# Kernel tuning notes

Measured on AMD Instinct MI355X. Metric: run time of the kernel, lower is better.

Reference implementation:

```python
import jax, jax.numpy as jnp
import numpy as np

B, NPG, FANOUT = 32, 1024, 4       # graphs, nodes per graph, tree fan-out
H = 128                            # x_size == h_size
NUM_LAYERS = 4
A, BCAPS = 8, 8                    # TreeCaps a, b
DCC, N_CLASSES = 16, 50
ROUTING_ITER = 3
TYPE_VOCAB, TOKEN_VOCAB = 1000, 30000
EPS = 1e-10


def _build_forest():
    # parent of node i (i>0) is (i-1)//FANOUT; node 0 is root. Same tree per graph.
    child = np.arange(1, NPG)
    parent = (child - 1) // FANOUT
    pos = ((child - 1) % FANOUT).astype(np.float32)           # position in parent's mailbox
    cnt = np.bincount(parent, minlength=NPG).astype(np.float32)
    k = cnt[parent]                                           # child count of each edge's parent
    denom = np.maximum(k - 1.0, 1.0)
    lw = np.where(k == 1.0, 1.0, (k - 1.0 - pos) / denom).astype(np.float32)
    rw = np.where(k == 1.0, 0.0, pos / denom).astype(np.float32)
    offs = (np.arange(B) * NPG)[:, None]
    src = (child[None, :] + offs).reshape(-1).astype(np.int32)
    dst = (parent[None, :] + offs).reshape(-1).astype(np.int32)
    return src, dst, np.tile(lw, B), np.tile(rw, B), np.tile(cnt > 0, B)


def setup_inputs() -> dict:
    key = jax.random.key(0)
    ks = jax.random.split(key, 9)
    src, dst, lw, rw, has_children = _build_forest()
    N = B * NPG
    u = lambda k, s: jax.random.uniform(k, s, jnp.float32, -0.1, 0.1)
    return {
        "type_ids": jax.random.randint(ks[0], (N,), 0, TYPE_VOCAB, dtype=jnp.int32),
        "token_ids": jax.random.randint(ks[1], (N,), 0, TOKEN_VOCAB, dtype=jnp.int32),
        "src": jnp.asarray(src), "dst": jnp.asarray(dst),
        "lw": jnp.asarray(lw), "rw": jnp.asarray(rw),
        "has_children": jnp.asarray(has_children),
        "type_emb": jax.random.normal(ks[2], (TYPE_VOCAB, H - H // 2), jnp.float32),
        "token_emb": jax.random.normal(ks[3], (TOKEN_VOCAB, H // 2), jnp.float32),
        "W_left": u(ks[4], (NUM_LAYERS, H, H)),
        "W_right": u(ks[5], (NUM_LAYERS, H, H)),
        "W_top": u(ks[6], (NUM_LAYERS, H, H)),
        "b_conv": u(ks[7], (NUM_LAYERS, H)),
        "Wjm": 0.01 * jax.random.normal(ks[8], (A * H, DCC, N_CLASSES, NUM_LAYERS), jnp.float32),
    }


def squash(x, axis=-1):
    sq = jnp.sum(x * x, axis=axis, keepdims=True)
    return x * (sq / (1.0 + sq) / (jnp.sqrt(sq + EPS) + 1e-8))


def _vts_routing(uu):
    # uu: [NPG, H, L]  (one graph's primary capsules)
    l2 = jnp.sum(uu.reshape(NPG, -1) ** 2, axis=1)
    _, top_b = jax.lax.top_k(l2, BCAPS)
    u_i = jax.lax.stop_gradient(uu[top_b].reshape(-1, NUM_LAYERS))  # [BCAPS*H, L]
    _, top_a = jax.lax.top_k(l2, A)
    v_j = uu[top_a].reshape(-1, NUM_LAYERS)                         # [A*H, L]
    alpha = jnp.zeros((BCAPS * H, A * H), uu.dtype)
    for _ in range(ROUTING_ITER):
        alpha = alpha + u_i @ v_j.T
        beta = jax.nn.softmax(alpha, axis=-1)
        v_j = beta.T @ u_i
    return squash(v_j)                                              # [A*H, L]


def _dynamic_routing(SC, Wjm):
    # SC: [B, A*H, L], Wjm: [A*H, DCC, S, L]
    v = jnp.einsum('ncsm,bnm->bnsc', Wjm, SC)
    v_stop = jax.lax.stop_gradient(v)
    delta = jnp.zeros(SC.shape[:2] + (N_CLASSES,), SC.dtype)
    z = None
    for r in range(ROUTING_ITER):
        gamma = jax.nn.softmax(delta, axis=-1)
        vv = v if r == ROUTING_ITER - 1 else v_stop
        z = squash(jnp.einsum('bns,bnsc->bsc', gamma, vv))
        if r < ROUTING_ITER - 1:
            delta = delta + jnp.einsum('bnsc,bsc->bns', v_stop, z)
    return z                                                        # [B, S, DCC]


def reference(type_ids, token_ids, src, dst, lw, rw, has_children,
              type_emb, token_emb, W_left, W_right, W_top, b_conv, Wjm):
    h = jnp.concatenate([type_emb[type_ids], token_emb[token_ids]], axis=1)  # [N, H]
    N = h.shape[0]
    feats = []
    for l in range(NUM_LAYERS):
        ch = h[src]                                                 # [E, H] gather children
        msg = (ch @ W_left[l]) * lw[:, None] + (ch @ W_right[l]) * rw[:, None]
        children = jax.ops.segment_sum(msg, dst, num_segments=N)
        new_h = jax.nn.relu(children + h @ W_top[l] + b_conv[l][None, :])
        h = jnp.where(has_children[:, None], new_h, h)              # leaves keep old h
        feats.append(h)
    layer_feats = jnp.stack(feats, axis=-1)                         # [N, H, L]
    SC = jax.vmap(_vts_routing)(layer_feats.reshape(B, NPG, H, NUM_LAYERS))
    z = _dynamic_routing(SC, Wjm)
    logit = jnp.sqrt(jnp.sum(z * z, axis=-1) + EPS)                 # [B, S]
    return (logit, logit)
```

## Files before the change

kernel.cpp:

```cpp
#include <hip/hip_runtime.h>


#define BG      32
#define NPG     1024
#define HH      128
#define NLAY    4
#define INT_PG  256
#define M_INT   8192
#define NN      32768
#define EPG     1023
#define DCC     16
#define NS      50

__global__ void k_embed(const int* __restrict__ tids, const int* __restrict__ kids,
                        const float* __restrict__ temb, const float* __restrict__ kemb,
                        float* __restrict__ h) {
  int idx = blockIdx.x * 256 + threadIdx.x;
  int n = idx >> 5, c4 = idx & 31;
  float4 v;
  if (c4 < 16) v = *(const float4*)(temb + tids[n] * 64 + c4 * 4);
  else         v = *(const float4*)(kemb + kids[n] * 64 + (c4 - 16) * 4);
  *(float4*)(h + n * 128 + c4 * 4) = v;
}

__global__ void k_gather(const float* __restrict__ h, const int* __restrict__ src,
                         const float* __restrict__ lw, const float* __restrict__ rw,
                         float* __restrict__ hl, float* __restrict__ hr) {
  int idx = blockIdx.x * 256 + threadIdx.x;
  int p = idx >> 5, c4 = idx & 31;
  int g = p >> 8, pl = p & 255;
  float4 al = make_float4(0.f, 0.f, 0.f, 0.f);
  float4 ar = make_float4(0.f, 0.f, 0.f, 0.f);
  for (int j = 0; j < 4; ++j) {
    int cc = 4 * pl + 1 + j;
    if (cc < NPG) {
      int e = g * EPG + cc - 1;
      int child = src[e];
      float lv = lw[e], rv = rw[e];
      float4 hv = *(const float4*)(h + child * 128 + c4 * 4);
      al.x = fmaf(lv, hv.x, al.x); al.y = fmaf(lv, hv.y, al.y);
      al.z = fmaf(lv, hv.z, al.z); al.w = fmaf(lv, hv.w, al.w);
      ar.x = fmaf(rv, hv.x, ar.x); ar.y = fmaf(rv, hv.y, ar.y);
      ar.z = fmaf(rv, hv.z, ar.z); ar.w = fmaf(rv, hv.w, ar.w);
    }
  }
  *(float4*)(hl + p * 128 + c4 * 4) = al;
  *(float4*)(hr + p * 128 + c4 * 4) = ar;
}

__global__ __launch_bounds__(256) void k_conv(
    const float* __restrict__ hl, const float* __restrict__ hr,
    float* __restrict__ h,
    const float* __restrict__ Wl, const float* __restrict__ Wr,
    const float* __restrict__ Wt, const float* __restrict__ bias,
    float* __restrict__ feat) {
  __shared__ float Ws[32][128];
  __shared__ float AsT[32][20];
  int tid = threadIdx.x;
  int tx = tid & 31, ty = tid >> 5;
  int rowBase = blockIdx.x * 16;
  int nodeBase = ((rowBase >> 8) << 10) + (rowBase & 255);
  float acc[2][4] = {};
  int sr = tid >> 3, sc4 = (tid & 7) * 4;

  for (int kc = 0; kc < 12; ++kc) {
    int ssel = kc >> 2, kcol = (kc & 3) * 32;
    const float* ap = (ssel == 0) ? (hl + rowBase * 128)
                    : (ssel == 1) ? (hr + rowBase * 128)
                                  : (h + nodeBase * 128);
    const float* wsrc = ((ssel == 0) ? Wl : (ssel == 1) ? Wr : Wt) + kcol * 128;
    float4 av = make_float4(0.f, 0.f, 0.f, 0.f);
    if (tid < 128) av = *(const float4*)(ap + sr * 128 + kcol + sc4);
    float4 wv0, wv1, wv2, wv3;
    {
      int f0 = tid, f1 = tid + 256, f2 = tid + 512, f3 = tid + 768;
      wv0 = *(const float4*)(wsrc + (f0 >> 5) * 128 + (f0 & 31) * 4);
      wv1 = *(const float4*)(wsrc + (f1 >> 5) * 128 + (f1 & 31) * 4);
      wv2 = *(const float4*)(wsrc + (f2 >> 5) * 128 + (f2 & 31) * 4);
      wv3 = *(const float4*)(wsrc + (f3 >> 5) * 128 + (f3 & 31) * 4);
    }
    __syncthreads();
    if (tid < 128) {
      AsT[sc4 + 0][sr] = av.x; AsT[sc4 + 1][sr] = av.y;
      AsT[sc4 + 2][sr] = av.z; AsT[sc4 + 3][sr] = av.w;
    }
    {
      int f0 = tid, f1 = tid + 256, f2 = tid + 512, f3 = tid + 768;
      *(float4*)&Ws[f0 >> 5][(f0 & 31) * 4] = wv0;
      *(float4*)&Ws[f1 >> 5][(f1 & 31) * 4] = wv1;
      *(float4*)&Ws[f2 >> 5][(f2 & 31) * 4] = wv2;
      *(float4*)&Ws[f3 >> 5][(f3 & 31) * 4] = wv3;
    }
    __syncthreads();
    #pragma unroll
    for (int kk = 0; kk < 32; ++kk) {
      float4 wv = *(float4*)&Ws[kk][tx * 4];
      float2 av2 = *(float2*)&AsT[kk][ty * 2];
      float aa[2] = {av2.x, av2.y};
      float ww[4] = {wv.x, wv.y, wv.z, wv.w};
      #pragma unroll
      for (int i = 0; i < 2; ++i)
        #pragma unroll
        for (int j = 0; j < 4; ++j)
          acc[i][j] = fmaf(aa[i], ww[j], acc[i][j]);
    }
  }
  float4 bv = *(const float4*)(bias + tx * 4);
  float bb[4] = {bv.x, bv.y, bv.z, bv.w};
  #pragma unroll
  for (int i = 0; i < 2; ++i) {
    int r = ty * 2 + i;
    float4 o = make_float4(fmaxf(acc[i][0] + bb[0], 0.f),
                           fmaxf(acc[i][1] + bb[1], 0.f),
                           fmaxf(acc[i][2] + bb[2], 0.f),
                           fmaxf(acc[i][3] + bb[3], 0.f));
    *(float4*)(feat + (rowBase + r) * 128 + tx * 4) = o;
    *(float4*)(h + (nodeBase + r) * 128 + tx * 4) = o;
  }
}

__global__ void k_l2(const float* __restrict__ h, const float* __restrict__ feat,
                     float* __restrict__ l2) {
  int wid = (blockIdx.x * 256 + threadIdx.x) >> 6;
  int lane = threadIdx.x & 63;
  int g = wid >> 10, local = wid & 1023;
  float s = 0.f;
  if (local >= INT_PG) {
    const float* p = h + wid * 128;
    float a = p[lane], b = p[lane + 64];
    s = (a * a + b * b) * 4.f;
  } else {
    int row = (g * INT_PG + local) * 128;
    #pragma unroll
    for (int l = 0; l < 4; ++l) {
      const float* p = feat + l * (M_INT * 128) + row;
      float a = p[lane], b = p[lane + 64];
      s += a * a + b * b;
    }
  }
  #pragma unroll
  for (int off = 32; off; off >>= 1) s += __shfl_down(s, off);
  if (lane == 0) l2[wid] = s;
}

__global__ __launch_bounds__(256) void k_topsel(const float* __restrict__ l2,
                                                const float* __restrict__ h,
                                                const float* __restrict__ feat,
                                                float* __restrict__ U,
                                                float* __restrict__ Vsum) {
  __shared__ int ssel[8];
  int g = blockIdx.x, tid = threadIdx.x;
  int lane = tid & 63;
  if (tid < 64) {
    unsigned long long kk[16];
    #pragma unroll
    for (int k = 0; k < 16; ++k) {
      int i = k * 64 + lane;
      unsigned vb = __float_as_uint(l2[g * 1024 + i]);
      kk[k] = ((unsigned long long)vb << 32) | (unsigned)(~i);
    }
    for (int r = 0; r < 8; ++r) {
      unsigned long long best = 0ULL;
      #pragma unroll
      for (int k = 0; k < 16; ++k) best = (kk[k] > best) ? kk[k] : best;
      #pragma unroll
      for (int off = 32; off; off >>= 1) {
        unsigned long long o = __shfl_down(best, off);
        best = (o > best) ? o : best;
      }
      best = __shfl(best, 0);
      if (lane == 0) ssel[r] = (int)(~(unsigned)(best & 0xffffffffu));
      #pragma unroll
      for (int k = 0; k < 16; ++k) if (kk[k] == best) kk[k] = 0ULL;
    }
  }
  __syncthreads();
  for (int t = 0; t < 4; ++t) {
    int idx = t * 256 + tid;
    int rank = idx >> 7, hh = idx & 127;
    int local = ssel[rank];
    float4 v;
    if (local >= INT_PG) {
      float x = h[(g * NPG + local) * 128 + hh];
      v = make_float4(x, x, x, x);
    } else {
      int row = (g * INT_PG + local) * 128 + hh;
      v.x = feat[row];
      v.y = feat[M_INT * 128 + row];
      v.z = feat[2 * M_INT * 128 + row];
      v.w = feat[3 * M_INT * 128 + row];
    }
    int o = g * 1024 + rank * 128 + hh;
    ((float4*)U)[o] = v;
    ((float4*)Vsum)[o] = v;
  }
}

__global__ __launch_bounds__(1024) void k_vtsA(const float* __restrict__ U,
                                               const float* __restrict__ Vsum,
                                               float* __restrict__ mw, float* __restrict__ sw) {
  __shared__ float4 Vs[1024];
  __shared__ float red[1024];
  int g = blockIdx.x >> 4, rb = (blockIdx.x & 15) * 64;
  int tid = threadIdx.x, l = tid & 63, p = tid >> 6;
  Vs[tid] = ((const float4*)Vsum)[g * 1024 + tid];
  __syncthreads();
  float4 u = ((const float4*)U)[g * 1024 + rb + l];
  int j0 = p * 64;
  float m = -3.4e38f;
  for (int j = j0; j < j0 + 64; ++j) {
    float4 v = Vs[j];
    float a = u.x * v.x + u.y * v.y + u.z * v.z + u.w * v.w;
    m = fmaxf(m, a);
  }
  red[tid] = m;
  __syncthreads();
  #pragma unroll
  for (int st = 512; st >= 64; st >>= 1) {
    if (tid < st) red[tid] = fmaxf(red[tid], red[tid + st]);
    __syncthreads();
  }
  float mm = red[l];
  __syncthreads();
  float s = 0.f;
  for (int j = j0; j < j0 + 64; ++j) {
    float4 v = Vs[j];
    float a = u.x * v.x + u.y * v.y + u.z * v.z + u.w * v.w;
    s += __expf(a - mm);
  }
  red[tid] = s;
  __syncthreads();
  #pragma unroll
  for (int st = 512; st >= 64; st >>= 1) {
    if (tid < st) red[tid] = red[tid] + red[tid + st];
    __syncthreads();
  }
  if (tid < 64) {
    mw[g * 1024 + rb + tid] = mm;
    sw[g * 1024 + rb + tid] = red[tid];
  }
}

__global__ __launch_bounds__(1024) void k_vtsB(const float* __restrict__ U,
                                               float* __restrict__ Vsum,
                                               const float* __restrict__ mw,
                                               const float* __restrict__ sw,
                                               float* __restrict__ SCT, int last) {
  __shared__ float4 Us[1024];
  __shared__ float2 ms[1024];
  __shared__ float4 par[1024];
  int g = blockIdx.x >> 4, cb = (blockIdx.x & 15) * 64;
  int tid = threadIdx.x, l = tid & 63, p = tid >> 6;
  Us[tid] = ((const float4*)U)[g * 1024 + tid];
  ms[tid] = make_float2(mw[g * 1024 + tid], 1.0f / sw[g * 1024 + tid]);
  __syncthreads();
  float4 v = ((const float4*)Vsum)[g * 1024 + cb + l];
  float4 acc = make_float4(0.f, 0.f, 0.f, 0.f);
  int i0 = p * 64;
  for (int i = i0; i < i0 + 64; ++i) {
    float4 uu = Us[i];
    float2 st = ms[i];
    float a = uu.x * v.x + uu.y * v.y + uu.z * v.z + uu.w * v.w;
    float w = __expf(a - st.x) * st.y;
    acc.x = fmaf(w, uu.x, acc.x); acc.y = fmaf(w, uu.y, acc.y);
    acc.z = fmaf(w, uu.z, acc.z); acc.w = fmaf(w, uu.w, acc.w);
  }
  par[tid] = acc;
  __syncthreads();
  #pragma unroll
  for (int st = 512; st >= 64; st >>= 1) {
    if (tid < st) {
      float4 a = par[tid], b = par[tid + st];
      par[tid] = make_float4(a.x + b.x, a.y + b.y, a.z + b.z, a.w + b.w);
    }
    __syncthreads();
  }
  if (tid < 64) {
    float4 o = par[tid];
    int jc = cb + tid;
    if (last) {
      float sq = o.x * o.x + o.y * o.y + o.z * o.z + o.w * o.w;
      float f = (sq / (1.f + sq)) / (sqrtf(sq + 1e-10f) + 1e-8f);
      ((float4*)SCT)[jc * 32 + g] = make_float4(o.x * f, o.y * f, o.z * f, o.w * f);
    } else {
      float4 w0 = ((const float4*)Vsum)[g * 1024 + jc];
      ((float4*)Vsum)[g * 1024 + jc] = make_float4(w0.x + o.x, w0.y + o.y,
                                                   w0.z + o.z, w0.w + o.w);
    }
  }
}

__global__ void k_transW(const float* __restrict__ Wjm, float* __restrict__ WT) {
  __shared__ float w[3200];
  int n = blockIdx.x, tid = threadIdx.x;
  for (int i = tid; i < 3200; i += 256) w[i] = Wjm[n * 3200 + i];
  __syncthreads();
  for (int i = tid; i < 3200; i += 256) {
    int s = i >> 6, cm = i & 63;
    int cc = cm >> 2, m = cm & 3;
    WT[(s * 1024 + n) * 64 + cm] = w[(cc * NS + s) * 4 + m];
  }
}

__global__ __launch_bounds__(256) void k_zsweep(const float* __restrict__ WT,
                                                const float* __restrict__ SCT,
                                                const float* __restrict__ gT,
                                                float* __restrict__ accZ, int it0) {
  int sb = blockIdx.x >> 4, nb = blockIdx.x & 15;
  int tid = threadIdx.x;
  int b = tid & 31, ch = tid >> 5;
  int n0 = nb * 64;
  const float4* wt = (const float4*)WT + (sb * 1024 + n0) * 16;
  const float4* sct = (const float4*)SCT + n0 * 32 + b;
  const float* gp = gT + (sb * 1024 + n0) * 32 + b;
  float a0 = 0.f, a1 = 0.f;
  #pragma unroll 4
  for (int nn = 0; nn < 64; ++nn) {
    float4 w0 = wt[nn * 16 + ch];
    float4 w1 = wt[nn * 16 + ch + 8];
    float4 s4 = sct[nn * 32];
    float gm = it0 ? (1.0f / 50.0f) : gp[nn * 32];
    float t0 = w0.x * s4.x + w0.y * s4.y + w0.z * s4.z + w0.w * s4.w;
    float t1 = w1.x * s4.x + w1.y * s4.y + w1.z * s4.z + w1.w * s4.w;
    a0 = fmaf(gm, t0, a0);
    a1 = fmaf(gm, t1, a1);
  }
  atomicAdd(accZ + (b * NS + sb) * 16 + ch, a0);
  atomicAdd(accZ + (b * NS + sb) * 16 + ch + 8, a1);
}

__global__ void k_logits(const float* __restrict__ accZ, float* __restrict__ out) {
  int idx = blockIdx.x * 256 + threadIdx.x;
  if (idx >= 1600) return;
  const float4* a4 = (const float4*)accZ + idx * 4;
  float4 u0 = a4[0], u1 = a4[1], u2 = a4[2], u3 = a4[3];
  float sq = u0.x * u0.x + u0.y * u0.y + u0.z * u0.z + u0.w * u0.w
           + u1.x * u1.x + u1.y * u1.y + u1.z * u1.z + u1.w * u1.w
           + u2.x * u2.x + u2.y * u2.y + u2.z * u2.z + u2.w * u2.w
           + u3.x * u3.x + u3.y * u3.y + u3.z * u3.z + u3.w * u3.w;
  float f = (sq / (1.f + sq)) / (sqrtf(sq + 1e-10f) + 1e-8f);
  float lg = sqrtf(sq * f * f + 1e-10f);
  out[idx] = lg;
  out[idx + 1600] = lg;
}

__global__ __launch_bounds__(256) void k_dsweep(const float* __restrict__ WT,
                                                const float* __restrict__ SCT,
                                                const float* __restrict__ accZ,
                                                float* __restrict__ delta,
                                                float* __restrict__ gT, int first) {
  __shared__ float wl[50 * 64];
  __shared__ float4 scl[32];
  __shared__ float dtot[NS][32];
  __shared__ float mb[32], ib[32];
  int n = blockIdx.x;
  int tid = threadIdx.x;
  for (int i = tid; i < 3200; i += 256)
    wl[i] = WT[((i >> 6) * 1024 + n) * 64 + (i & 63)];
  if (tid < 32) scl[tid] = ((const float4*)SCT)[n * 32 + tid];
  __syncthreads();
  for (int idx = tid; idx < 1600; idx += 256) {
    int s = idx >> 5, b = idx & 31;
    const float4* wp = (const float4*)(wl + s * 64);
    const float4* zp = (const float4*)(accZ + (b * 50 + s) * 16);
    float4 u0 = zp[0], u1 = zp[1], u2 = zp[2], u3 = zp[3];
    float sq = u0.x * u0.x + u0.y * u0.y + u0.z * u0.z + u0.w * u0.w
             + u1.x * u1.x + u1.y * u1.y + u1.z * u1.z + u1.w * u1.w
             + u2.x * u2.x + u2.y * u2.y + u2.z * u2.z + u2.w * u2.w
             + u3.x * u3.x + u3.y * u3.y + u3.z * u3.z + u3.w * u3.w;
    float f = (sq / (1.f + sq)) / (sqrtf(sq + 1e-10f) + 1e-8f);
    float zs[16] = {u0.x * f, u0.y * f, u0.z * f, u0.w * f,
                    u1.x * f, u1.y * f, u1.z * f, u1.w * f,
                    u2.x * f, u2.y * f, u2.z * f, u2.w * f,
                    u3.x * f, u3.y * f, u3.z * f, u3.w * f};
    float4 y = make_float4(0.f, 0.f, 0.f, 0.f);
    #pragma unroll
    for (int c = 0; c < 16; ++c) {
      float4 w = wp[c];
      float zc = zs[c];
      y.x = fmaf(zc, w.x, y.x); y.y = fmaf(zc, w.y, y.y);
      y.z = fmaf(zc, w.z, y.z); y.w = fmaf(zc, w.w, y.w);
    }
    float4 sc = scl[b];
    float dd = sc.x * y.x + sc.y * y.y + sc.z * y.z + sc.w * y.w;
    float dt = first ? dd : (delta[(s * 1024 + n) * 32 + b] + dd);
    dtot[s][b] = dt;
    if (first) delta[(s * 1024 + n) * 32 + b] = dt;
  }
  __syncthreads();
  if (tid < 32) {
    float m = -3.4e38f;
    for (int s = 0; s < NS; ++s) m = fmaxf(m, dtot[s][tid]);
    float sum = 0.f;
    for (int s = 0; s < NS; ++s) sum += __expf(dtot[s][tid] - m);
    mb[tid] = m; ib[tid] = 1.0f / sum;
  }
  __syncthreads();
  for (int idx = tid; idx < 1600; idx += 256) {
    int s = idx >> 5, b = idx & 31;
    gT[(s * 1024 + n) * 32 + b] = __expf(dtot[s][b] - mb[b]) * ib[b];
  }
}

extern "C" void kernel_launch(void* const* d_in, const int* in_sizes, int n_in,
                              void* d_out, int out_size, void* d_ws, size_t ws_size,
                              hipStream_t stream) {
  const int*   type_ids  = (const int*)d_in[0];
  const int*   token_ids = (const int*)d_in[1];
  const int*   src       = (const int*)d_in[2];
  const float* lw        = (const float*)d_in[4];
  const float* rw        = (const float*)d_in[5];
  const float* temb      = (const float*)d_in[7];
  const float* kemb      = (const float*)d_in[8];
  const float* Wl        = (const float*)d_in[9];
  const float* Wr        = (const float*)d_in[10];
  const float* Wt        = (const float*)d_in[11];
  const float* bconv     = (const float*)d_in[12];
  const float* Wjm       = (const float*)d_in[13];
  float* out = (float*)d_out;
  char* wsb = (char*)d_ws;

  float* h     = (float*)(wsb + 0);
  float* feat  = (float*)(wsb + 16777216);
  float* WT    = (float*)(wsb + 33554432);
  float* delta = (float*)(wsb + 46661632);
  float* gT    = (float*)(wsb + 53215232);
  float* accZ  = (float*)(wsb + 59768832);
  float* l2b   = (float*)(wsb + 60076032);
  float* U     = (float*)(wsb + 60207104);
  float* Vsum  = (float*)(wsb + 60731392);
  float* mw    = (float*)(wsb + 61255680);
  float* sw    = (float*)(wsb + 61386752);
  float* SCT   = (float*)(wsb + 61517824);
  float* hl    = (float*)(wsb + 62042112);
  float* hr    = (float*)(wsb + 66236416);

  k_embed<<<4096, 256, 0, stream>>>(type_ids, token_ids, temb, kemb, h);
  k_transW<<<1024, 256, 0, stream>>>(Wjm, WT);
  hipMemsetAsync(accZ, 0, 3 * 32 * 50 * 16 * 4, stream);

  for (int l = 0; l < NLAY; ++l) {
    k_gather<<<1024, 256, 0, stream>>>(h, src, lw, rw, hl, hr);
    k_conv<<<512, 256, 0, stream>>>(hl, hr, h,
                                    Wl + l * 16384, Wr + l * 16384, Wt + l * 16384,
                                    bconv + l * 128, feat + l * (M_INT * 128));
  }

  k_l2<<<8192, 256, 0, stream>>>(h, feat, l2b);
  k_topsel<<<32, 256, 0, stream>>>(l2b, h, feat, U, Vsum);

  for (int it = 0; it < 3; ++it) {
    k_vtsA<<<512, 1024, 0, stream>>>(U, Vsum, mw, sw);
    k_vtsB<<<512, 1024, 0, stream>>>(U, Vsum, mw, sw, SCT, it == 2 ? 1 : 0);
  }

  for (int it = 0; it < 3; ++it) {
    float* aZ = accZ + it * 25600;
    k_zsweep<<<800, 256, 0, stream>>>(WT, SCT, gT, aZ, it == 0 ? 1 : 0);
    if (it < 2)
      k_dsweep<<<1024, 256, 0, stream>>>(WT, SCT, aZ, delta, gT, it == 0 ? 1 : 0);
  }
  k_logits<<<7, 256, 0, stream>>>(accZ + 2 * 25600, out);
}
```

Before: 476.3 us.

## Fuse child gather into conv kernel with ping-pong h buffers and double-buffered tiles

Removes the separate gather kernel by computing the weighted left/right child sums directly into shared memory inside the conv kernel. This drops the hl/hr global round trip and one launch per layer. Because blocks now read children that other blocks overwrite, h is ping-ponged between two buffers. Leaf rows are copied into both buffers at embed time so unchanged nodes stay valid. The GEMM K-loop also double-buffers its weight and activation tiles, halving barriers, at the cost of more shared memory per block.

Result: no change. 477.1 us (+0.2%).

```diff
diff --git a/kernel.cpp b/kernel.cpp
--- a/kernel.cpp
+++ b/kernel.cpp
@@ -14,88 +14,113 @@
 
 __global__ void k_embed(const int* __restrict__ tids, const int* __restrict__ kids,
                         const float* __restrict__ temb, const float* __restrict__ kemb,
-                        float* __restrict__ h) {
+                        float* __restrict__ hA, float* __restrict__ hB) {
   int idx = blockIdx.x * 256 + threadIdx.x;
   int n = idx >> 5, c4 = idx & 31;
   float4 v;
   if (c4 < 16) v = *(const float4*)(temb + tids[n] * 64 + c4 * 4);
   else         v = *(const float4*)(kemb + kids[n] * 64 + (c4 - 16) * 4);
-  *(float4*)(h + n * 128 + c4 * 4) = v;
-}
-
-__global__ void k_gather(const float* __restrict__ h, const int* __restrict__ src,
-                         const float* __restrict__ lw, const float* __restrict__ rw,
-                         float* __restrict__ hl, float* __restrict__ hr) {
-  int idx = blockIdx.x * 256 + threadIdx.x;
-  int p = idx >> 5, c4 = idx & 31;
-  int g = p >> 8, pl = p & 255;
-  float4 al = make_float4(0.f, 0.f, 0.f, 0.f);
-  float4 ar = make_float4(0.f, 0.f, 0.f, 0.f);
-  for (int j = 0; j < 4; ++j) {
-    int cc = 4 * pl + 1 + j;
-    if (cc < NPG) {
-      int e = g * EPG + cc - 1;
-      int child = src[e];
-      float lv = lw[e], rv = rw[e];
-      float4 hv = *(const float4*)(h + child * 128 + c4 * 4);
-      al.x = fmaf(lv, hv.x, al.x); al.y = fmaf(lv, hv.y, al.y);
-      al.z = fmaf(lv, hv.z, al.z); al.w = fmaf(lv, hv.w, al.w);
-      ar.x = fmaf(rv, hv.x, ar.x); ar.y = fmaf(rv, hv.y, ar.y);
-      ar.z = fmaf(rv, hv.z, ar.z); ar.w = fmaf(rv, hv.w, ar.w);
-    }
-  }
-  *(float4*)(hl + p * 128 + c4 * 4) = al;
-  *(float4*)(hr + p * 128 + c4 * 4) = ar;
+  *(float4*)(hA + n * 128 + c4 * 4) = v;
+  if ((n & 1023) >= INT_PG)
+    *(float4*)(hB + n * 128 + c4 * 4) = v;
 }
 
 __global__ __launch_bounds__(256) void k_conv(
-    const float* __restrict__ hl, const float* __restrict__ hr,
-    float* __restrict__ h,
+    const float* __restrict__ hp, float* __restrict__ hn,
+    const int* __restrict__ src, const float* __restrict__ lw,
+    const float* __restrict__ rw,
     const float* __restrict__ Wl, const float* __restrict__ Wr,
     const float* __restrict__ Wt, const float* __restrict__ bias,
     float* __restrict__ feat) {
-  __shared__ float Ws[32][128];
-  __shared__ float AsT[32][20];
+  __shared__ float Ws[2][32][128];
+  __shared__ float AsT[2][32][20];
+  __shared__ float hlS[16][128];
+  __shared__ float hrS[16][128];
   int tid = threadIdx.x;
   int tx = tid & 31, ty = tid >> 5;
   int rowBase = blockIdx.x * 16;
-  int nodeBase = ((rowBase >> 8) << 10) + (rowBase & 255);
+  int g = rowBase >> 8, plBase = rowBase & 255;
+  int nodeBase = g * NPG + plBase;
+
+  #pragma unroll
+  for (int t = 0; t < 2; ++t) {
+    int it = t * 256 + tid;
+    int pw = it >> 5, c4 = it & 31;
+    int pl = plBase + pw;
+    float4 al = make_float4(0.f, 0.f, 0.f, 0.f);
+    float4 ar = make_float4(0.f, 0.f, 0.f, 0.f);
+    #pragma unroll
+    for (int j = 0; j < 4; ++j) {
+      int cc = 4 * pl + 1 + j;
+      if (cc < NPG) {
+        int e = g * EPG + cc - 1;
+        int child = src[e];
+        float lv = lw[e], rv = rw[e];
+        float4 hv = *(const float4*)(hp + child * 128 + c4 * 4);
+        al.x = fmaf(lv, hv.x, al.x); al.y = fmaf(lv, hv.y, al.y);
+        al.z = fmaf(lv, hv.z, al.z); al.w = fmaf(lv, hv.w, al.w);
+        ar.x = fmaf(rv, hv.x, ar.x); ar.y = fmaf(rv, hv.y, ar.y);
+        ar.z = fmaf(rv, hv.z, ar.z); ar.w = fmaf(rv, hv.w, ar.w);
+      }
+    }
+    *(float4*)&hlS[pw][c4 * 4] = al;
+    *(float4*)&hrS[pw][c4 * 4] = ar;
+  }
+  __syncthreads();
+
   float acc[2][4] = {};
   int sr = tid >> 3, sc4 = (tid & 7) * 4;
 
+  {
+    float4 av = make_float4(0.f, 0.f, 0.f, 0.f);
+    if (tid < 128) av = *(const float4*)&hlS[sr][sc4];
+    const float* wsrc = Wl;
+    int f0 = tid, f1 = tid + 256, f2 = tid + 512, f3 = tid + 768;
+    float4 wv0 = *(const float4*)(wsrc + (f0 >> 5) * 128 + (f0 & 31) * 4);
+    float4 wv1 = *(const float4*)(wsrc + (f1 >> 5) * 128 + (f1 & 31) * 4);
+    float4 wv2 = *(const float4*)(wsrc + (f2 >> 5) * 128 + (f2 & 31) * 4);
+    float4 wv3 = *(const float4*)(wsrc + (f3 >> 5) * 128 + (f3 & 31) * 4);
+    if (tid < 128) {
+      AsT[0][sc4 + 0][sr] = av.x; AsT[0][sc4 + 1][sr] = av.y;
+      AsT[0][sc4 + 2][sr] = av.z; AsT[0][sc4 + 3][sr] = av.w;
+    }
+    *(float4*)&Ws[0][f0 >> 5][(f0 & 31) * 4] = wv0;
+    *(float4*)&Ws[0][f1 >> 5][(f1 & 31) * 4] = wv1;
+    *(float4*)&Ws[0][f2 >> 5][(f2 & 31) * 4] = wv2;
+    *(float4*)&Ws[0][f3 >> 5][(f3 & 31) * 4] = wv3;
+  }
+  __syncthreads();
+
   for (int kc = 0; kc < 12; ++kc) {
-    int ssel = kc >> 2, kcol = (kc & 3) * 32;
-    const float* ap = (ssel == 0) ? (hl + rowBase * 128)
-                    : (ssel == 1) ? (hr + rowBase * 128)
-                                  : (h + nodeBase * 128);
-    const float* wsrc = ((ssel == 0) ? Wl : (ssel == 1) ? Wr : Wt) + kcol * 128;
-    float4 av = make_float4(0.f, 0.f, 0.f, 0.f);
-    if (tid < 128) av = *(const float4*)(ap + sr * 128 + kcol + sc4);
-    float4 wv0, wv1, wv2, wv3;
-    {
+    int cur = kc & 1, nxt = cur ^ 1;
+    if (kc < 11) {
+      int kc1 = kc + 1;
+      int ssel = kc1 >> 2, kcol = (kc1 & 3) * 32;
+      float4 av = make_float4(0.f, 0.f, 0.f, 0.f);
+      if (tid < 128) {
+        if (ssel == 0)      av = *(const float4*)&hlS[sr][kcol + sc4];
+        else if (ssel == 1) av = *(const float4*)&hrS[sr][kcol + sc4];
+        else                av = *(const float4*)(hp + (nodeBase + sr) * 128 + kcol + sc4);
+      }
+      const float* wsrc = ((ssel == 0) ? Wl : (ssel == 1) ? Wr : Wt) + kcol * 128;
       int f0 = tid, f1 = tid + 256, f2 = tid + 512, f3 = tid + 768;
-      wv0 = *(const float4*)(wsrc + (f0 >> 5) * 128 + (f0 & 31) * 4);
-      wv1 = *(const float4*)(wsrc + (f1 >> 5) * 128 + (f1 & 31) * 4);
-      wv2 = *(const float4*)(wsrc + (f2 >> 5) * 128 + (f2 & 31) * 4);
-      wv3 = *(const float4*)(wsrc + (f3 >> 5) * 128 + (f3 & 31) * 4);
-    }
-    __syncthreads();
-    if (tid < 128) {
-      AsT[sc4 + 0][sr] = av.x; AsT[sc4 + 1][sr] = av.y;
-      AsT[sc4 + 2][sr] = av.z; AsT[sc4 + 3][sr] = av.w;
-    }
-    {
-      int f0 = tid, f1 = tid + 256, f2 = tid + 512, f3 = tid + 768;
-      *(float4*)&Ws[f0 >> 5][(f0 & 31) * 4] = wv0;
-      *(float4*)&Ws[f1 >> 5][(f1 & 31) * 4] = wv1;
-      *(float4*)&Ws[f2 >> 5][(f2 & 31) * 4] = wv2;
-      *(float4*)&Ws[f3 >> 5][(f3 & 31) * 4] = wv3;
-    }
-    __syncthreads();
+      float4 wv0 = *(const float4*)(wsrc + (f0 >> 5) * 128 + (f0 & 31) * 4);
+      float4 wv1 = *(const float4*)(wsrc + (f1 >> 5) * 128 + (f1 & 31) * 4);
+      float4 wv2 = *(const float4*)(wsrc + (f2 >> 5) * 128 + (f2 & 31) * 4);
+      float4 wv3 = *(const float4*)(wsrc + (f3 >> 5) * 128 + (f3 & 31) * 4);
+      if (tid < 128) {
+        AsT[nxt][sc4 + 0][sr] = av.x; AsT[nxt][sc4 + 1][sr] = av.y;
+        AsT[nxt][sc4 + 2][sr] = av.z; AsT[nxt][sc4 + 3][sr] = av.w;
+      }
+      *(float4*)&Ws[nxt][f0 >> 5][(f0 & 31) * 4] = wv0;
+      *(float4*)&Ws[nxt][f1 >> 5][(f1 & 31) * 4] = wv1;
+      *(float4*)&Ws[nxt][f2 >> 5][(f2 & 31) * 4] = wv2;
+      *(float4*)&Ws[nxt][f3 >> 5][(f3 & 31) * 4] = wv3;
+    }
     #pragma unroll
     for (int kk = 0; kk < 32; ++kk) {
-      float4 wv = *(float4*)&Ws[kk][tx * 4];
-      float2 av2 = *(float2*)&AsT[kk][ty * 2];
+      float4 wv = *(float4*)&Ws[cur][kk][tx * 4];
+      float2 av2 = *(float2*)&AsT[cur][kk][ty * 2];
       float aa[2] = {av2.x, av2.y};
       float ww[4] = {wv.x, wv.y, wv.z, wv.w};
       #pragma unroll
@@ -104,6 +129,7 @@
         for (int j = 0; j < 4; ++j)
           acc[i][j] = fmaf(aa[i], ww[j], acc[i][j]);
     }
+    if (kc != 11) __syncthreads();
   }
   float4 bv = *(const float4*)(bias + tx * 4);
   float bb[4] = {bv.x, bv.y, bv.z, bv.w};
@@ -115,7 +141,7 @@
                            fmaxf(acc[i][2] + bb[2], 0.f),
                            fmaxf(acc[i][3] + bb[3], 0.f));
     *(float4*)(feat + (rowBase + r) * 128 + tx * 4) = o;
-    *(float4*)(h + (nodeBase + r) * 128 + tx * 4) = o;
+    *(float4*)(hn + (nodeBase + r) * 128 + tx * 4) = o;
   }
 }
 
@@ -420,34 +446,34 @@
   float* out = (float*)d_out;
   char* wsb = (char*)d_ws;
 
-  float* h     = (float*)(wsb + 0);
-  float* feat  = (float*)(wsb + 16777216);
-  float* WT    = (float*)(wsb + 33554432);
-  float* delta = (float*)(wsb + 46661632);
-  float* gT    = (float*)(wsb + 53215232);
-  float* accZ  = (float*)(wsb + 59768832);
-  float* l2b   = (float*)(wsb + 60076032);
-  float* U     = (float*)(wsb + 60207104);
-  float* Vsum  = (float*)(wsb + 60731392);
-  float* mw    = (float*)(wsb + 61255680);
-  float* sw    = (float*)(wsb + 61386752);
-  float* SCT   = (float*)(wsb + 61517824);
-  float* hl    = (float*)(wsb + 62042112);
-  float* hr    = (float*)(wsb + 66236416);
-
-  k_embed<<<4096, 256, 0, stream>>>(type_ids, token_ids, temb, kemb, h);
+  float* hA    = (float*)(wsb + 0);
+  float* hB    = (float*)(wsb + 16777216);
+  float* feat  = (float*)(wsb + 33554432);
+  float* WT    = (float*)(wsb + 50331648);
+  float* delta = (float*)(wsb + 63438848);
+  float* gT    = (float*)(wsb + 69992448);
+  float* accZ  = (float*)(wsb + 76546048);
+  float* l2b   = (float*)(wsb + 76853248);
+  float* U     = (float*)(wsb + 76984320);
+  float* Vsum  = (float*)(wsb + 77508608);
+  float* mw    = (float*)(wsb + 78032896);
+  float* sw    = (float*)(wsb + 78163968);
+  float* SCT   = (float*)(wsb + 78295040);
+
+  k_embed<<<4096, 256, 0, stream>>>(type_ids, token_ids, temb, kemb, hA, hB);
   k_transW<<<1024, 256, 0, stream>>>(Wjm, WT);
   hipMemsetAsync(accZ, 0, 3 * 32 * 50 * 16 * 4, stream);
 
   for (int l = 0; l < NLAY; ++l) {
-    k_gather<<<1024, 256, 0, stream>>>(h, src, lw, rw, hl, hr);
-    k_conv<<<512, 256, 0, stream>>>(hl, hr, h,
+    const float* hp = (l & 1) ? hB : hA;
+    float*       hn = (l & 1) ? hA : hB;
+    k_conv<<<512, 256, 0, stream>>>(hp, hn, src, lw, rw,
                                     Wl + l * 16384, Wr + l * 16384, Wt + l * 16384,
                                     bconv + l * 128, feat + l * (M_INT * 128));
   }
 
-  k_l2<<<8192, 256, 0, stream>>>(h, feat, l2b);
-  k_topsel<<<32, 256, 0, stream>>>(l2b, h, feat, U, Vsum);
+  k_l2<<<8192, 256, 0, stream>>>(hA, feat, l2b);
+  k_topsel<<<32, 256, 0, stream>>>(l2b, hA, feat, U, Vsum);
 
   for (int it = 0; it < 3; ++it) {
     k_vtsA<<<512, 1024, 0, stream>>>(U, Vsum, mw, sw);
```
